# Kernel optimization log

Hardware: AMD Instinct MI355X
Metric: run time of the kernel (lower is better)

## Reference

```python
import jax, jax.numpy as jnp
import numpy as np

EPS = 1e-5
NEG_SLOPE = 0.2

def _bn(x, g, b, m, v):
    # eval-mode BatchNorm over channel axis 1
    sh = (1, -1) + (1,) * (x.ndim - 2)
    inv = g.reshape(sh) * jax.lax.rsqrt(v.reshape(sh) + EPS)
    return (x - m.reshape(sh)) * inv + b.reshape(sh)

def _lrelu(x):
    return jnp.where(x >= 0, x, NEG_SLOPE * x)

def _edge_feature(x, idx):
    # x: [B,C,N], idx: [B,N,k] -> edge diffs [B,C,N,k]
    xT = jnp.transpose(x, (0, 2, 1))                      # [B,N,C]
    B = x.shape[0]
    neigh = xT[jnp.arange(B)[:, None, None], idx]         # [B,N,k,C]
    e = neigh - xT[:, :, None, :]                         # [B,N,k,C]
    return jnp.transpose(e, (0, 3, 1, 2))                 # [B,C,N,k]

def _edgeconv(x, idx, w, g, b, m, v):
    e = _edge_feature(x, idx)                             # [B,Cin,N,k]
    y = jnp.einsum('bcnk,oc->bonk', e, w)                 # 1x1 conv2d, no bias
    y = _lrelu(_bn(y, g, b, m, v))
    return jnp.max(y, axis=-1)                            # max over k -> [B,Cout,N]

def _pointconv(x, w, g, b, m, v):
    y = jnp.einsum('bcn,oc->bon', x, w)                   # 1x1 conv1d, no bias
    return _lrelu(_bn(y, g, b, m, v))

def setup_inputs() -> dict:
    key = jax.random.key(0)
    B, N, K = 8, 4096, 20
    ks = jax.random.split(key, 40)
    it = iter(range(40))
    d = {}
    d['x'] = jax.random.normal(ks[next(it)], (B, 3, N), dtype=jnp.float32)
    d['idx'] = jax.random.randint(ks[next(it)], (B, N, K), 0, N, dtype=jnp.int32)
    dims = [(64, 3), (64, 64), (128, 64), (256, 128), (256, 512), (128, 256), (1, 128)]
    for i, (o, c) in enumerate(dims, 1):
        d[f'w{i}'] = jax.random.normal(ks[next(it)], (o, c), dtype=jnp.float32) * (1.0 / np.sqrt(c))
    for i, c in enumerate([64, 64, 128, 256, 256, 128], 1):
        d[f'g{i}'] = jax.random.uniform(ks[next(it)], (c,), dtype=jnp.float32, minval=0.5, maxval=1.5)
        d[f'b{i}'] = jax.random.normal(ks[next(it)], (c,), dtype=jnp.float32) * 0.1
        d[f'm{i}'] = jax.random.normal(ks[next(it)], (c,), dtype=jnp.float32) * 0.1
        d[f'v{i}'] = jax.random.uniform(ks[next(it)], (c,), dtype=jnp.float32, minval=0.5, maxval=1.5)
    return d

def reference(x, idx, w1, w2, w3, w4, w5, w6, w7,
              g1, b1, m1, v1, g2, b2, m2, v2, g3, b3, m3, v3,
              g4, b4, m4, v4, g5, b5, m5, v5, g6, b6, m6, v6):
    x1 = _edgeconv(x,  idx, w1, g1, b1, m1, v1)   # [B,64,N]
    x2 = _edgeconv(x1, idx, w2, g2, b2, m2, v2)   # [B,64,N]
    x3 = _edgeconv(x2, idx, w3, g3, b3, m3, v3)   # [B,128,N]
    x4 = _edgeconv(x3, idx, w4, g4, b4, m4, v4)   # [B,256,N]
    h = jnp.concatenate((x1, x2, x3, x4), axis=1) # [B,512,N]
    h = _pointconv(h, w5, g5, b5, m5, v5)         # [B,256,N]
    h = _pointconv(h, w6, g6, b6, m6, v6)         # [B,128,N]
    h = _lrelu(jnp.einsum('bcn,oc->bon', h, w7))  # [B,1,N]
    return jnp.transpose(h, (0, 2, 1))            # [B,N,1]
```

## Files before the change

kernel.cpp:

```cpp
#include <hip/hip_runtime.h>
#include <hip/hip_bf16.h>
#include <cstdint>
#include <cstddef>

#define EPS 1e-5f
#define NEG 0.2f

static constexpr int B_ = 8, N_ = 4096, K_ = 20, M_ = B_ * N_;

typedef __attribute__((ext_vector_type(8))) _Float16 f16x8;
typedef __attribute__((ext_vector_type(4))) float f32x4;

#define VMCNT(n) asm volatile("s_waitcnt vmcnt(" #n ")" ::: "memory")

__device__ __forceinline__ void gload_lds16(const _Float16* g, _Float16* l) {
  __builtin_amdgcn_global_load_lds(
      (const __attribute__((address_space(1))) uint32_t*)g,
      (__attribute__((address_space(3))) uint32_t*)l, 16, 0, 0);
}

__global__ __launch_bounds__(256) void prep_c3(
    const float* __restrict__ x, const float* __restrict__ w1,
    const float* __restrict__ w2, const float* __restrict__ w3,
    const float* __restrict__ w4, const float* __restrict__ w5,
    const float* __restrict__ w6,
    const float* __restrict__ g1, const float* __restrict__ b1, const float* __restrict__ m1, const float* __restrict__ v1,
    const float* __restrict__ g2, const float* __restrict__ b2, const float* __restrict__ m2, const float* __restrict__ v2,
    const float* __restrict__ g3, const float* __restrict__ b3, const float* __restrict__ m3, const float* __restrict__ v3,
    const float* __restrict__ g4, const float* __restrict__ b4, const float* __restrict__ m4, const float* __restrict__ v4,
    const float* __restrict__ g5, const float* __restrict__ b5, const float* __restrict__ m5, const float* __restrict__ v5,
    const float* __restrict__ g6, const float* __restrict__ b6, const float* __restrict__ m6, const float* __restrict__ v6,
    float* __restrict__ P, _Float16* __restrict__ Wh, _Float16* __restrict__ z) {
  const int bid = blockIdx.x, tid = threadIdx.x;
  if (bid < 512) {
    const int o  = tid & 63;
    const int pi = tid >> 6;
    const float ww0 = w1[o * 3 + 0], ww1 = w1[o * 3 + 1], ww2 = w1[o * 3 + 2];
    const float iv = g1[o] * rsqrtf(v1[o] + EPS);
    const int pbase = bid * 64;
    const int b = pbase >> 12;
    const int nbase = pbase & (N_ - 1);
    const float* xb = x + (size_t)b * 3 * N_;
    for (int pj = pi; pj < 64; pj += 4) {
      const int n = nbase + pj;
      const float x0 = xb[n], x1v = xb[N_ + n], x2v = xb[2 * N_ + n];
      z[(size_t)(pbase + pj) * 64 + o] = (_Float16)((x0 * ww0 + x1v * ww1 + x2v * ww2) * iv);
    }
    return;
  }
  if (bid == 1328) {
    const float* G[6]  = {g1, g2, g3, g4, g5, g6};
    const float* Bb[6] = {b1, b2, b3, b4, b5, b6};
    const float* Mm[6] = {m1, m2, m3, m4, m5, m6};
    const float* Vv[6] = {v1, v2, v3, v4, v5, v6};
    const int Cs[6] = {64, 64, 128, 256, 256, 128};
    const int OI[6] = {0, 128, 256, 512, 1024, 1536};
    const int OB[6] = {64, 192, 384, 768, 1280, 1664};
    for (int l = 0; l < 6; ++l) {
      for (int c = tid; c < Cs[l]; c += 256) {
        float iv = G[l][c] * rsqrtf(Vv[l][c] + EPS);
        P[OI[l] + c] = iv;
        P[OB[l] + c] = Bb[l][c] - Mm[l][c] * iv;
      }
    }
    return;
  }
  const int fb = bid - 512;
  const float* w; const float* g; const float* v; _Float16* dst; int lc, base;
  if (fb < 16)       { w = w2; g = g2; v = v2; dst = Wh + 0;      lc = 6; base = 0;   }
  else if (fb < 48)  { w = w3; g = g3; v = v3; dst = Wh + 4096;   lc = 6; base = 16;  }
  else if (fb < 176) { w = w4; g = g4; v = v4; dst = Wh + 12288;  lc = 7; base = 48;  }
  else if (fb < 688) { w = w5; g = g5; v = v5; dst = Wh + 45056;  lc = 9; base = 176; }
  else               { w = w6; g = g6; v = v6; dst = Wh + 176128; lc = 8; base = 688; }
  const int e = (fb - base) * 256 + tid;
  const int o = e >> lc;
  dst[e] = (_Float16)(w[e] * (g[o] * rsqrtf(v[o] + EPS)));
}

template <int BO>
__global__ __launch_bounds__(256) void edge_gemm64(
    const _Float16* __restrict__ z, const int* __restrict__ idx,
    const float* __restrict__ betap,
    const _Float16* __restrict__ W,
    _Float16* __restrict__ hout,
    _Float16* __restrict__ zout, int ldzout) {
  constexpr int GW = BO / 8;
  constexpr int OJ = BO / 32;
  __shared__ _Float16 Asmem[128 * 64];
  __shared__ _Float16 Wsmem[BO * 64];

  const int tid = threadIdx.x, lane = tid & 63, wid = tid >> 6;
  const int batch = blockIdx.x & 7, chunk = blockIdx.x >> 3;
  const int bm0 = (batch << 12) + chunk * 128;
  const int lr = lane & 15, lk = lane >> 4;

  const _Float16* Wbase = W + (size_t)lr * 64 + lk * 8;
#pragma unroll
  for (int g = wid; g < GW; g += 4) {
    const int o = g >> 1, s = g & 1;
    gload_lds16(Wbase + (size_t)16 * o * 64 + s * 32, Wsmem + g * 512);
  }

  const int lid = tid & 7, cb = lid * 8;
  float bt[8];
#pragma unroll
  for (int q = 0; q < 8; ++q) bt[q] = betap[cb + q];
  const _Float16* zb = z + ((size_t)(batch << 12)) * 64;
#pragma unroll
  for (int pass = 0; pass < 4; ++pass) {
    const int pi = pass * 32 + (tid >> 3);
    const int p = bm0 + pi;
    const int* ip = idx + (size_t)p * K_;
    const int ir0 = ip[lid];
    const int ir1 = ip[8 + lid];
    const int ir2 = ip[16 + (lid & 3)];
    f16x8 mx = *reinterpret_cast<const f16x8*>(zb + (size_t)__shfl(ir0, 0, 8) * 64 + cb);
#pragma unroll
    for (int k = 1; k < K_; ++k) {
      const int g = (k < 8) ? __shfl(ir0, k, 8)
                  : (k < 16) ? __shfl(ir1, k - 8, 8)
                             : __shfl(ir2, k - 16, 8);
      const f16x8 v = *reinterpret_cast<const f16x8*>(zb + (size_t)g * 64 + cb);
#pragma unroll
      for (int q = 0; q < 8; ++q) mx[q] = v[q] > mx[q] ? v[q] : mx[q];
    }
    const f16x8 vc = *reinterpret_cast<const f16x8*>(z + (size_t)p * 64 + cb);
    f16x8 vo;
#pragma unroll
    for (int q = 0; q < 8; ++q) {
      const float e = (float)mx[q] - (float)vc[q] + bt[q];
      vo[q] = (_Float16)fmaxf(e, NEG * e);
    }
    *reinterpret_cast<f16x8*>(hout + (size_t)p * 512 + cb) = vo;
    const int i = pi >> 4, rr = pi & 15, s = cb >> 5, kk = (cb >> 3) & 3;
    *reinterpret_cast<f16x8*>(Asmem + (i * 2 + s) * 512 + ((kk << 4) | rr) * 8) = vo;
  }
  __syncthreads();

  const int wr = wid >> 1, wc = wid & 1;
  f32x4 acc[4][OJ];
#pragma unroll
  for (int i = 0; i < 4; ++i)
#pragma unroll
    for (int j = 0; j < OJ; ++j) acc[i][j] = (f32x4){0.f, 0.f, 0.f, 0.f};
#pragma unroll
  for (int s = 0; s < 2; ++s) {
    f16x8 av[4], wv[OJ];
#pragma unroll
    for (int i = 0; i < 4; ++i)
      av[i] = *reinterpret_cast<const f16x8*>(Asmem + ((wr * 4 + i) * 2 + s) * 512 + lane * 8);
#pragma unroll
    for (int j = 0; j < OJ; ++j)
      wv[j] = *reinterpret_cast<const f16x8*>(Wsmem + ((wc * OJ + j) * 2 + s) * 512 + lane * 8);
#pragma unroll
    for (int i = 0; i < 4; ++i)
#pragma unroll
      for (int j = 0; j < OJ; ++j)
        acc[i][j] = __builtin_amdgcn_mfma_f32_16x16x32_f16(av[i], wv[j], acc[i][j], 0, 0, 0);
  }

#pragma unroll
  for (int j = 0; j < OJ; ++j) {
    const int o = wc * (BO / 2) + 16 * j + lr;
#pragma unroll
    for (int i = 0; i < 4; ++i) {
      const int r0 = bm0 + wr * 64 + 16 * i + lk * 4;
#pragma unroll
      for (int q = 0; q < 4; ++q)
        zout[(size_t)(r0 + q) * ldzout + o] = (_Float16)acc[i][j][q];
    }
  }
}

__global__ __launch_bounds__(512, 1) void edge_gemm_l4(
    const _Float16* __restrict__ z3,
    const int* __restrict__ idx,
    const float* __restrict__ btE,
    const _Float16* __restrict__ W4,
    _Float16* __restrict__ h512,
    _Float16* __restrict__ z4out) {
  constexpr int SB = 24 * 512;
  __shared__ _Float16 lds[4 * SB];

  const int tid = threadIdx.x, lane = tid & 63, wid = tid >> 6;
  const int wr = wid >> 2, wc = wid & 3;
  const int bid = blockIdx.x, batch = bid & 7;
  const int bm0 = (batch << 12) + (bid >> 3) * 128;
  const int lr = lane & 15, lk = lane >> 4;

  const _Float16* Wb = W4 + (size_t)lr * 128 + lk * 8;
#pragma unroll
  for (int q = 0; q < 8; ++q) {
    const int gg = wid * 8 + q;
    const int ob = gg >> 2, kk = gg & 3;
    gload_lds16(Wb + (size_t)16 * ob * 128 + kk * 32, &lds[kk * SB + (8 + ob) * 512]);
  }

  const int lid = tid & 15, cb = lid * 8;
  float bt[8];
#pragma unroll
  for (int q = 0; q < 8; ++q) bt[q] = btE[cb + q];
  const _Float16* zb = z3 + ((size_t)(batch << 12)) * 128;
  f16x8 x3r[4];
#pragma unroll
  for (int pass = 0; pass < 4; ++pass) {
    const int pi = pass * 32 + (tid >> 4);
    const int p = bm0 + pi;
    const int* ip = idx + (size_t)p * K_;
    const int ir0 = ip[lid];
    const int ir1 = (lid < 4) ? ip[16 + lid] : 0;
    f16x8 mx = *reinterpret_cast<const f16x8*>(zb + (size_t)__shfl(ir0, 0, 16) * 128 + cb);
#pragma unroll
    for (int k = 1; k < K_; ++k) {
      const int g = (k < 16) ? __shfl(ir0, k, 16) : __shfl(ir1, k - 16, 16);
      const f16x8 v = *reinterpret_cast<const f16x8*>(zb + (size_t)g * 128 + cb);
#pragma unroll
      for (int q = 0; q < 8; ++q) mx[q] = v[q] > mx[q] ? v[q] : mx[q];
    }
    const f16x8 vc = *reinterpret_cast<const f16x8*>(z3 + (size_t)p * 128 + cb);
    f16x8 vo;
#pragma unroll
    for (int q = 0; q < 8; ++q) {
      const float e = (float)mx[q] - (float)vc[q] + bt[q];
      vo[q] = (_Float16)fmaxf(e, NEG * e);
    }
    x3r[pass] = vo;
    *reinterpret_cast<f16x8*>(h512 + (size_t)p * 512 + 128 + cb) = vo;
  }
  {
    const int kk = (cb >> 3) & 3;
    const int ts = cb >> 5;
    const int rr = (tid >> 4) & 15;
#pragma unroll
    for (int pp = 0; pp < 4; ++pp) {
      const int grp = pp * 2 + (tid >> 8);
      *reinterpret_cast<f16x8*>(&lds[ts * SB + grp * 512 + ((kk << 4) | rr) * 8]) = x3r[pp];
    }
  }
  __syncthreads();

  f32x4 acc[4][4];
#pragma unroll
  for (int i = 0; i < 4; ++i)
#pragma unroll
    for (int j = 0; j < 4; ++j) acc[i][j] = (f32x4){0.f, 0.f, 0.f, 0.f};
#pragma unroll
  for (int t = 0; t < 4; ++t) {
    f16x8 av[4], wv[4];
#pragma unroll
    for (int i = 0; i < 4; ++i)
      av[i] = *reinterpret_cast<const f16x8*>(&lds[t * SB + (wr * 4 + i) * 512 + lane * 8]);
#pragma unroll
    for (int j = 0; j < 4; ++j)
      wv[j] = *reinterpret_cast<const f16x8*>(&lds[t * SB + (8 + wc * 4 + j) * 512 + lane * 8]);
#pragma unroll
    for (int i = 0; i < 4; ++i)
#pragma unroll
      for (int j = 0; j < 4; ++j)
        acc[i][j] = __builtin_amdgcn_mfma_f32_16x16x32_f16(av[i], wv[j], acc[i][j], 0, 0, 0);
  }

#pragma unroll
  for (int j = 0; j < 4; ++j) {
    const int o = wc * 64 + 16 * j + lr;
#pragma unroll
    for (int i = 0; i < 4; ++i) {
      const int r0 = bm0 + wr * 64 + 16 * i + lk * 4;
#pragma unroll
      for (int q = 0; q < 4; ++q)
        z4out[(size_t)(r0 + q) * 256 + o] = (_Float16)acc[i][j][q];
    }
  }
}

template <int O>
__global__ __launch_bounds__(256) void edge_max8(
    const _Float16* __restrict__ z, const int* __restrict__ idx,
    const float* __restrict__ betap, _Float16* __restrict__ out, int ldout) {
  constexpr int TPP = O / 8;
  constexpr int PPB = 256 / TPP;
  constexpr int NW = (K_ + TPP - 1) / TPP;
  const int t = threadIdx.x;
  const int batch = blockIdx.x & 7;
  const int chunk = blockIdx.x >> 3;
  const int p = (batch << 12) + chunk * PPB + t / TPP;
  const int lid = t % TPP;
  const int cb = lid * 8;
  const int* ip = idx + (size_t)p * K_;
  int ir[NW];
#pragma unroll
  for (int wv = 0; wv < NW; ++wv) {
    const int l = wv * TPP + lid;
    ir[wv] = (l < K_) ? ip[l] : ip[0];
  }
  const _Float16* zb = z + ((size_t)(batch << 12)) * O;

  f16x8 mx = *reinterpret_cast<const f16x8*>(zb + (size_t)__shfl(ir[0], 0, TPP) * O + cb);
#pragma unroll
  for (int k = 1; k < K_; ++k) {
    const int g = __shfl(ir[k / TPP], k % TPP, TPP);
    const f16x8 v = *reinterpret_cast<const f16x8*>(zb + (size_t)g * O + cb);
#pragma unroll
    for (int q = 0; q < 8; ++q) mx[q] = v[q] > mx[q] ? v[q] : mx[q];
  }
  const f16x8 vc = *reinterpret_cast<const f16x8*>(z + (size_t)p * O + cb);
  f16x8 vo;
#pragma unroll
  for (int q = 0; q < 8; ++q) {
    const float e = (float)mx[q] - (float)vc[q] + betap[cb + q];
    vo[q] = (_Float16)fmaxf(e, NEG * e);
  }
  *reinterpret_cast<f16x8*>(out + (size_t)p * ldout + cb) = vo;
}

template <int BM, int BO, int C, int MODE>
__global__ __launch_bounds__(512, 1) void gemm_pipe8(
    const _Float16* __restrict__ A, int lda,
    const _Float16* __restrict__ W,
    const float* __restrict__ betap,
    _Float16* __restrict__ out, int ldout,
    const float* __restrict__ w7, float* __restrict__ dout) {
  constexpr int NK = C / 32;
  constexpr int GA = BM / 16;
  constexpr int GW = BO / 16;
  constexpr int GT = GA + GW;
  constexpr int GP = GT / 8;
  constexpr int SB = (BM + BO) * 32;
  constexpr int MI = BM / 32;
  constexpr int OJ = BO / 64;
  __shared__ _Float16 lds[4 * SB];

  const int lane = threadIdx.x & 63;
  const int wid  = threadIdx.x >> 6;
  const int wr = wid >> 2, wc = wid & 3;
  const int bid = blockIdx.x;
  const int bm0 = ((bid & 7) << 12) + (bid >> 3) * BM;
  const int lr = lane & 15, lk = lane >> 4;

  const _Float16* Abase = A + (size_t)(bm0 + lr) * lda + lk * 8;
  const _Float16* Wbase = W + (size_t)lr * C + lk * 8;

  f32x4 acc[MI][OJ];
#pragma unroll
  for (int i = 0; i < MI; ++i)
#pragma unroll
    for (int j = 0; j < OJ; ++j) acc[i][j] = (f32x4){0.f, 0.f, 0.f, 0.f};

  auto stage = [&](int buf, int k0) {
    _Float16* dst = &lds[buf * SB];
#pragma unroll
    for (int q = 0; q < GP; ++q) {
      const int g = wid * GP + q;
      const _Float16* src = (g < GA)
          ? Abase + (size_t)16 * g * lda + k0
          : Wbase + (size_t)16 * (g - GA) * C + k0;
      gload_lds16(src, dst + g * 512);
    }
  };

  auto compute = [&](int buf) {
    const _Float16* Ab = &lds[buf * SB];
    const _Float16* Wb2 = &lds[buf * SB + GA * 512];
    f16x8 av[MI], wv[OJ];
#pragma unroll
    for (int i = 0; i < MI; ++i)
      av[i] = *reinterpret_cast<const f16x8*>(Ab + (wr * MI + i) * 512 + lane * 8);
#pragma unroll
    for (int j = 0; j < OJ; ++j)
      wv[j] = *reinterpret_cast<const f16x8*>(Wb2 + (wc * OJ + j) * 512 + lane * 8);
#pragma unroll
    for (int i = 0; i < MI; ++i)
#pragma unroll
      for (int j = 0; j < OJ; ++j)
        acc[i][j] = __builtin_amdgcn_mfma_f32_16x16x32_f16(av[i], wv[j], acc[i][j], 0, 0, 0);
  };

  stage(0, 0);
  stage(1, 32);
#pragma unroll
  for (int t = 0; t < NK; ++t) {
    if (t + 2 < NK) {
      stage((t + 2) & 3, (t + 2) * 32);
      if constexpr (GP == 2)      VMCNT(4);
      else                        VMCNT(6);
    } else if (t + 1 < NK) {
      if constexpr (GP == 2)      VMCNT(2);
      else                        VMCNT(3);
    } else {
      VMCNT(0);
    }
    __builtin_amdgcn_s_barrier();
    compute(t & 3);
  }

  if constexpr (MODE == 2) {
    __shared__ float dotbuf[BM][4];
    float rowdot[MI][4];
#pragma unroll
    for (int i = 0; i < MI; ++i)
#pragma unroll
      for (int q = 0; q < 4; ++q) rowdot[i][q] = 0.f;
#pragma unroll
    for (int j = 0; j < OJ; ++j) {
      const int o = wc * (BO / 4) + 16 * j + lr;
      const float bt = betap[o];
      const float wf = w7[o];
#pragma unroll
      for (int i = 0; i < MI; ++i)
#pragma unroll
        for (int q = 0; q < 4; ++q) {
          float t = acc[i][j][q] + bt;
          t = fmaxf(t, NEG * t);
          rowdot[i][q] += t * wf;
        }
    }
#pragma unroll
    for (int i = 0; i < MI; ++i)
#pragma unroll
      for (int q = 0; q < 4; ++q) {
#pragma unroll
        for (int off = 1; off < 16; off <<= 1)
          rowdot[i][q] += __shfl_xor(rowdot[i][q], off, 16);
        if (lr == 0) dotbuf[wr * (BM / 2) + 16 * i + lk * 4 + q][wc] = rowdot[i][q];
      }
    __syncthreads();
    if (threadIdx.x < BM) {
      const float s = dotbuf[threadIdx.x][0] + dotbuf[threadIdx.x][1] +
                      dotbuf[threadIdx.x][2] + dotbuf[threadIdx.x][3];
      dout[bm0 + threadIdx.x] = fmaxf(s, NEG * s);
    }
    return;
  }

#pragma unroll
  for (int j = 0; j < OJ; ++j) {
    const int o = wc * (BO / 4) + 16 * j + lr;
    const float bt = betap[o];
#pragma unroll
    for (int i = 0; i < MI; ++i) {
      const int r0 = bm0 + wr * (BM / 2) + 16 * i + lk * 4;
#pragma unroll
      for (int q = 0; q < 4; ++q) {
        float t = acc[i][j][q] + bt;
        t = fmaxf(t, NEG * t);
        out[(size_t)(r0 + q) * ldout + o] = (_Float16)t;
      }
    }
  }
}

extern "C" void kernel_launch(void* const* d_in, const int* in_sizes, int n_in,
                              void* d_out, int out_size, void* d_ws, size_t ws_size,
                              hipStream_t stream) {
  const float* x  = (const float*)d_in[0];
  const int* idx  = (const int*)d_in[1];
  const float* w[7];
  for (int i = 0; i < 7; ++i) w[i] = (const float*)d_in[2 + i];
  const float* bn[24];
  for (int i = 0; i < 24; ++i) bn[i] = (const float*)d_in[9 + i];

  float* P       = (float*)d_ws;
  _Float16* Wh   = (_Float16*)((char*)d_ws + (32 << 10));
  _Float16* z_a  = (_Float16*)((char*)d_ws + (1u << 20));
  _Float16* h512 = (_Float16*)((char*)d_ws + (17u << 20));
  _Float16* z_b  = (_Float16*)((char*)d_ws + (49u << 20));

  prep_c3<<<1329, 256, 0, stream>>>(
      x, w[0], w[1], w[2], w[3], w[4], w[5],
      bn[0], bn[1], bn[2], bn[3],   bn[4], bn[5], bn[6], bn[7],
      bn[8], bn[9], bn[10], bn[11], bn[12], bn[13], bn[14], bn[15],
      bn[16], bn[17], bn[18], bn[19], bn[20], bn[21], bn[22], bn[23],
      P, Wh, z_a);

  const float* bt1 = P + 64;
  const float* bt2 = P + 192;
  const float* bt3 = P + 384;
  const float* bt4 = P + 768;
  const float* bt5 = P + 1280;
  const float* bt6 = P + 1664;
  const _Float16* W2 = Wh + 0, *W3 = Wh + 4096, *W4 = Wh + 12288,
               *W5 = Wh + 45056, *W6 = Wh + 176128;

  edge_gemm64<64><<<M_ / 128, 256, 0, stream>>>(z_a, idx, bt1, W2, h512 + 0, z_b, 64);
  edge_gemm64<128><<<M_ / 128, 256, 0, stream>>>(z_b, idx, bt2, W3, h512 + 64, z_a, 128);
  edge_gemm_l4<<<M_ / 128, 512, 0, stream>>>(z_a, idx, bt3, W4, h512, z_b);
  edge_max8<256><<<M_ / 8, 256, 0, stream>>>(z_b, idx, bt4, h512 + 256, 512);
  gemm_pipe8<128, 256, 512, 1><<<M_ / 128, 512, 0, stream>>>(
      h512, 512, W5, bt5, z_a, 256, nullptr, nullptr);
  gemm_pipe8<128, 128, 256, 2><<<M_ / 128, 512, 0, stream>>>(
      z_a, 256, W6, bt6, nullptr, 0, w[6], (float*)d_out);
}
```

Before: 104.2 us.

## Fuse pointconv layers 5, 6 and final dot into one LDS-resident GEMM kernel

```diff
diff --git a/kernel.cpp b/kernel.cpp
--- a/kernel.cpp
+++ b/kernel.cpp
@@ -313,139 +313,159 @@
   *reinterpret_cast<f16x8*>(out + (size_t)p * ldout + cb) = vo;
 }
 
-template <int BM, int BO, int C, int MODE>
-__global__ __launch_bounds__(512, 1) void gemm_pipe8(
-    const _Float16* __restrict__ A, int lda,
-    const _Float16* __restrict__ W,
-    const float* __restrict__ betap,
-    _Float16* __restrict__ out, int ldout,
-    const float* __restrict__ w7, float* __restrict__ dout) {
-  constexpr int NK = C / 32;
-  constexpr int GA = BM / 16;
-  constexpr int GW = BO / 16;
-  constexpr int GT = GA + GW;
-  constexpr int GP = GT / 8;
-  constexpr int SB = (BM + BO) * 32;
-  constexpr int MI = BM / 32;
-  constexpr int OJ = BO / 64;
-  __shared__ _Float16 lds[4 * SB];
-
-  const int lane = threadIdx.x & 63;
-  const int wid  = threadIdx.x >> 6;
+__global__ __launch_bounds__(512, 1) void gemm_l567(
+    const _Float16* __restrict__ A,
+    const _Float16* __restrict__ W5,
+    const float* __restrict__ bt5,
+    const _Float16* __restrict__ W6,
+    const float* __restrict__ bt6,
+    const float* __restrict__ w7,
+    float* __restrict__ dout) {
+  constexpr int SB = 24 * 512;
+  constexpr int H5 = 4 * SB;
+  __shared__ _Float16 lds[4 * SB + 32768];
+
+  const int tid = threadIdx.x, lane = tid & 63, wid = tid >> 6;
   const int wr = wid >> 2, wc = wid & 3;
   const int bid = blockIdx.x;
-  const int bm0 = ((bid & 7) << 12) + (bid >> 3) * BM;
+  const int bm0 = ((bid & 7) << 12) + (bid >> 3) * 128;
   const int lr = lane & 15, lk = lane >> 4;
 
-  const _Float16* Abase = A + (size_t)(bm0 + lr) * lda + lk * 8;
-  const _Float16* Wbase = W + (size_t)lr * C + lk * 8;
-
-  f32x4 acc[MI][OJ];
-#pragma unroll
-  for (int i = 0; i < MI; ++i)
-#pragma unroll
-    for (int j = 0; j < OJ; ++j) acc[i][j] = (f32x4){0.f, 0.f, 0.f, 0.f};
+  const _Float16* Abase = A + (size_t)(bm0 + lr) * 512 + lk * 8;
+  const _Float16* W5b = W5 + (size_t)lr * 512 + lk * 8;
+
+  f32x4 acc[4][4];
+#pragma unroll
+  for (int i = 0; i < 4; ++i)
+#pragma unroll
+    for (int j = 0; j < 4; ++j) acc[i][j] = (f32x4){0.f, 0.f, 0.f, 0.f};
 
   auto stage = [&](int buf, int k0) {
     _Float16* dst = &lds[buf * SB];
 #pragma unroll
-    for (int q = 0; q < GP; ++q) {
-      const int g = wid * GP + q;
-      const _Float16* src = (g < GA)
-          ? Abase + (size_t)16 * g * lda + k0
-          : Wbase + (size_t)16 * (g - GA) * C + k0;
+    for (int q = 0; q < 3; ++q) {
+      const int g = wid * 3 + q;
+      const _Float16* src = (g < 8)
+          ? Abase + (size_t)16 * g * 512 + k0
+          : W5b + (size_t)16 * (g - 8) * 512 + k0;
       gload_lds16(src, dst + g * 512);
     }
-  };
-
-  auto compute = [&](int buf) {
-    const _Float16* Ab = &lds[buf * SB];
-    const _Float16* Wb2 = &lds[buf * SB + GA * 512];
-    f16x8 av[MI], wv[OJ];
-#pragma unroll
-    for (int i = 0; i < MI; ++i)
-      av[i] = *reinterpret_cast<const f16x8*>(Ab + (wr * MI + i) * 512 + lane * 8);
-#pragma unroll
-    for (int j = 0; j < OJ; ++j)
-      wv[j] = *reinterpret_cast<const f16x8*>(Wb2 + (wc * OJ + j) * 512 + lane * 8);
-#pragma unroll
-    for (int i = 0; i < MI; ++i)
-#pragma unroll
-      for (int j = 0; j < OJ; ++j)
-        acc[i][j] = __builtin_amdgcn_mfma_f32_16x16x32_f16(av[i], wv[j], acc[i][j], 0, 0, 0);
   };
 
   stage(0, 0);
   stage(1, 32);
 #pragma unroll
-  for (int t = 0; t < NK; ++t) {
-    if (t + 2 < NK) {
+  for (int t = 0; t < 16; ++t) {
+    if (t + 2 < 16) {
       stage((t + 2) & 3, (t + 2) * 32);
-      if constexpr (GP == 2)      VMCNT(4);
-      else                        VMCNT(6);
-    } else if (t + 1 < NK) {
-      if constexpr (GP == 2)      VMCNT(2);
-      else                        VMCNT(3);
+      VMCNT(6);
+    } else if (t + 1 < 16) {
+      VMCNT(3);
     } else {
       VMCNT(0);
     }
     __builtin_amdgcn_s_barrier();
-    compute(t & 3);
-  }
-
-  if constexpr (MODE == 2) {
-    __shared__ float dotbuf[BM][4];
-    float rowdot[MI][4];
-#pragma unroll
-    for (int i = 0; i < MI; ++i)
-#pragma unroll
-      for (int q = 0; q < 4; ++q) rowdot[i][q] = 0.f;
-#pragma unroll
-    for (int j = 0; j < OJ; ++j) {
-      const int o = wc * (BO / 4) + 16 * j + lr;
-      const float bt = betap[o];
-      const float wf = w7[o];
-#pragma unroll
-      for (int i = 0; i < MI; ++i)
-#pragma unroll
-        for (int q = 0; q < 4; ++q) {
-          float t = acc[i][j][q] + bt;
-          t = fmaxf(t, NEG * t);
-          rowdot[i][q] += t * wf;
-        }
-    }
-#pragma unroll
-    for (int i = 0; i < MI; ++i)
+    const _Float16* Ab = &lds[(t & 3) * SB];
+    f16x8 av[4], wv[4];
+#pragma unroll
+    for (int i = 0; i < 4; ++i)
+      av[i] = *reinterpret_cast<const f16x8*>(Ab + (wr * 4 + i) * 512 + lane * 8);
+#pragma unroll
+    for (int j = 0; j < 4; ++j)
+      wv[j] = *reinterpret_cast<const f16x8*>(Ab + (8 + wc * 4 + j) * 512 + lane * 8);
+#pragma unroll
+    for (int i = 0; i < 4; ++i)
+#pragma unroll
+      for (int j = 0; j < 4; ++j)
+        acc[i][j] = __builtin_amdgcn_mfma_f32_16x16x32_f16(av[i], wv[j], acc[i][j], 0, 0, 0);
+  }
+
+  {
+    const _Float16* W6b = W6 + (size_t)lr * 256 + lk * 8;
+#pragma unroll
+    for (int q = 0; q < 8; ++q) {
+      const int gg = wid * 8 + q;
+      const int ob = gg >> 3, kk = gg & 7;
+      gload_lds16(W6b + (size_t)16 * ob * 256 + kk * 32, &lds[gg * 512]);
+    }
+  }
+#pragma unroll
+  for (int j = 0; j < 4; ++j) {
+    const int o = wc * 64 + 16 * j + lr;
+    const float b5 = bt5[o];
+    const int gcol = o >> 5;
+    const int slotc = (o >> 3) & 3;
+    const int elem = o & 7;
+#pragma unroll
+    for (int i = 0; i < 4; ++i) {
+      const int rg = wr * 4 + i;
 #pragma unroll
       for (int q = 0; q < 4; ++q) {
-#pragma unroll
-        for (int off = 1; off < 16; off <<= 1)
-          rowdot[i][q] += __shfl_xor(rowdot[i][q], off, 16);
-        if (lr == 0) dotbuf[wr * (BM / 2) + 16 * i + lk * 4 + q][wc] = rowdot[i][q];
+        const int rl = lk * 4 + q;
+        float t = acc[i][j][q] + b5;
+        t = fmaxf(t, NEG * t);
+        lds[H5 + (rg * 8 + gcol) * 512 + (slotc * 16 + rl) * 8 + elem] = (_Float16)t;
       }
-    __syncthreads();
-    if (threadIdx.x < BM) {
-      const float s = dotbuf[threadIdx.x][0] + dotbuf[threadIdx.x][1] +
-                      dotbuf[threadIdx.x][2] + dotbuf[threadIdx.x][3];
-      dout[bm0 + threadIdx.x] = fmaxf(s, NEG * s);
-    }
-    return;
-  }
-
-#pragma unroll
-  for (int j = 0; j < OJ; ++j) {
-    const int o = wc * (BO / 4) + 16 * j + lr;
-    const float bt = betap[o];
-#pragma unroll
-    for (int i = 0; i < MI; ++i) {
-      const int r0 = bm0 + wr * (BM / 2) + 16 * i + lk * 4;
+    }
+  }
+  __syncthreads();
+
+  f32x4 acc2[4][2];
+#pragma unroll
+  for (int i = 0; i < 4; ++i)
+#pragma unroll
+    for (int j = 0; j < 2; ++j) acc2[i][j] = (f32x4){0.f, 0.f, 0.f, 0.f};
+#pragma unroll
+  for (int t = 0; t < 8; ++t) {
+    f16x8 av[4], wv[2];
+#pragma unroll
+    for (int i = 0; i < 4; ++i)
+      av[i] = *reinterpret_cast<const f16x8*>(&lds[H5 + ((wr * 4 + i) * 8 + t) * 512 + lane * 8]);
+#pragma unroll
+    for (int j = 0; j < 2; ++j)
+      wv[j] = *reinterpret_cast<const f16x8*>(&lds[((wc * 2 + j) * 8 + t) * 512 + lane * 8]);
+#pragma unroll
+    for (int i = 0; i < 4; ++i)
+#pragma unroll
+      for (int j = 0; j < 2; ++j)
+        acc2[i][j] = __builtin_amdgcn_mfma_f32_16x16x32_f16(av[i], wv[j], acc2[i][j], 0, 0, 0);
+  }
+
+  float* dotbuf = (float*)&lds[32768];
+  float rowdot[4][4];
+#pragma unroll
+  for (int i = 0; i < 4; ++i)
+#pragma unroll
+    for (int q = 0; q < 4; ++q) rowdot[i][q] = 0.f;
+#pragma unroll
+  for (int j = 0; j < 2; ++j) {
+    const int o = wc * 32 + 16 * j + lr;
+    const float bt = bt6[o];
+    const float wf = w7[o];
+#pragma unroll
+    for (int i = 0; i < 4; ++i)
 #pragma unroll
       for (int q = 0; q < 4; ++q) {
-        float t = acc[i][j][q] + bt;
+        float t = acc2[i][j][q] + bt;
         t = fmaxf(t, NEG * t);
-        out[(size_t)(r0 + q) * ldout + o] = (_Float16)t;
+        rowdot[i][q] += t * wf;
       }
-    }
+  }
+#pragma unroll
+  for (int i = 0; i < 4; ++i)
+#pragma unroll
+    for (int q = 0; q < 4; ++q) {
+#pragma unroll
+      for (int off = 1; off < 16; off <<= 1)
+        rowdot[i][q] += __shfl_xor(rowdot[i][q], off, 16);
+      if (lr == 0)
+        dotbuf[(wr * 64 + 16 * i + lk * 4 + q) * 4 + wc] = rowdot[i][q];
+    }
+  __syncthreads();
+  if (tid < 128) {
+    const float s = dotbuf[tid * 4 + 0] + dotbuf[tid * 4 + 1] +
+                    dotbuf[tid * 4 + 2] + dotbuf[tid * 4 + 3];
+    dout[bm0 + tid] = fmaxf(s, NEG * s);
   }
 }
 
@@ -485,8 +505,6 @@
   edge_gemm64<128><<<M_ / 128, 256, 0, stream>>>(z_b, idx, bt2, W3, h512 + 64, z_a, 128);
   edge_gemm_l4<<<M_ / 128, 512, 0, stream>>>(z_a, idx, bt3, W4, h512, z_b);
   edge_max8<256><<<M_ / 8, 256, 0, stream>>>(z_b, idx, bt4, h512 + 256, 512);
-  gemm_pipe8<128, 256, 512, 1><<<M_ / 128, 512, 0, stream>>>(
-      h512, 512, W5, bt5, z_a, 256, nullptr, nullptr);
-  gemm_pipe8<128, 128, 256, 2><<<M_ / 128, 512, 0, stream>>>(
-      z_a, 256, W6, bt6, nullptr, 0, w[6], (float*)d_out);
-}
+  gemm_l567<<<M_ / 128, 512, 0, stream>>>(
+      h512, W5, bt5, W6, bt6, w[6], (float*)d_out);
+}
```

Result: faster. 90.61 us (-13.0%).
